# Kernel optimization log

Measured on AMD Instinct MI355X. Metric: run time of the kernel, lower is better.

Reference implementation:

```python
import jax, jax.numpy as jnp
import numpy as np

FREQ_CUTOFF = 10.0
SAMPLING_RATE = 100.0
FILTER_TYPE = 'lowpass'

B, C, L = 64, 128, 8192


def setup_inputs() -> dict:
    key = jax.random.key(0)
    x = jax.random.normal(key, (B, C, L), dtype=jnp.float32)
    return {"x": x}


def reference(x):
    # x: [B, C, L]
    seq_len = x.shape[-1]
    x_fft = jnp.fft.fft(x, axis=-1)  # complex64 [B, C, L]
    freqs = jnp.fft.fftfreq(seq_len, 1.0 / SAMPLING_RATE)  # [L]
    if FILTER_TYPE == 'lowpass':
        mask = jnp.abs(freqs) < FREQ_CUTOFF
    elif FILTER_TYPE == 'highpass':
        mask = jnp.abs(freqs) > FREQ_CUTOFF
    else:
        raise ValueError('Invalid filter type: {}'.format(FILTER_TYPE))
    # Zero out masked frequency bins (faithful to original: lowpass zeroes |f| < cutoff)
    x_fft = jnp.where(mask[None, None, :], 0.0 + 0.0j, x_fft)
    x_filtered = jnp.real(jnp.fft.ifft(x_fft, axis=-1)).astype(jnp.float32)
    return x_filtered
```

## Files before the change

### kernel.cpp

```cpp
#include <hip/hip_runtime.h>
#include <hip/hip_fp16.h>


#define FFT_N 8192
#define NT    256
#define PHY(i) ((i) + ((i) >> 6))

typedef float v2f __attribute__((ext_vector_type(2)));

__device__ __forceinline__ v2f cmul(v2f a, v2f b){
  v2f axx = {a.x, a.x};
  v2f ayy = {a.y, a.y};
  v2f byx = {-b.y, b.x};
  return axx * b + ayy * byx;
}

__device__ __forceinline__ v2f mul_w32(v2f d, int j, bool cj){
  if (j == 0) return d;
  if (j == 8) return cj ? (v2f){-d.y, d.x} : (v2f){d.y, -d.x};
  const float C[16] = {1.f, 0.98078528f, 0.92387953f, 0.83146961f, 0.70710678f,
                       0.55557023f, 0.38268343f, 0.19509032f, 0.f, -0.19509032f,
                       -0.38268343f, -0.55557023f, -0.70710678f, -0.83146961f,
                       -0.92387953f, -0.98078528f};
  const float S[16] = {0.f, -0.19509032f, -0.38268343f, -0.55557023f, -0.70710678f,
                       -0.83146961f, -0.92387953f, -0.98078528f, -1.f, -0.98078528f,
                       -0.92387953f, -0.83146961f, -0.70710678f, -0.55557023f,
                       -0.38268343f, -0.19509032f};
  v2f w = {C[j], cj ? -S[j] : S[j]};
  return cmul(d, w);
}

template<int SZ, int L>
__device__ __forceinline__ void dif_rec(v2f* r){
  #pragma unroll
  for (int g = 0; g < SZ; g += 2*L){
    #pragma unroll
    for (int j = 0; j < L; ++j){
      v2f u = r[g+j], v = r[g+j+L];
      r[g+j]   = u + v;
      r[g+j+L] = mul_w32(u - v, j*(16/L), false);
    }
  }
  if constexpr (L > 1) dif_rec<SZ, L/2>(r);
}

template<int SZ, int L>
__device__ __forceinline__ void dit_rec(v2f* r){
  #pragma unroll
  for (int g = 0; g < SZ; g += 2*L){
    #pragma unroll
    for (int j = 0; j < L; ++j){
      v2f a = r[g+j];
      v2f b = mul_w32(r[g+j+L], j*(16/L), true);
      r[g+j]   = a + b;
      r[g+j+L] = a - b;
    }
  }
  if constexpr (2*L < SZ) dit_rec<SZ, 2*L>(r);
}

__host__ __device__ constexpr int brev5(int k){
  return ((k&1)<<4) | ((k&2)<<2) | (k&4) | ((k&8)>>2) | ((k&16)>>4);
}

__device__ __forceinline__ void twiddle_scale(v2f* r, int cbase, bool cj){
  float s, c;
  __sincosf((float)cbase * -7.6699039394282061e-4f, &s, &c);
  if (cj) s = -s;
  const v2f w1 = {c, s};
  v2f w2q = cmul(w1, w1);
  v2f w4q = cmul(w2q, w2q);
  v2f w8q = cmul(w4q, w4q);
  v2f w16 = cmul(w8q, w8q);
  v2f wa = w1;
  r[brev5(1)]  = cmul(r[brev5(1)],  wa);
  r[brev5(17)] = cmul(r[brev5(17)], cmul(w16, wa));
  #pragma unroll
  for (int k = 2; k <= 15; ++k){
    wa = cmul(wa, w1);
    r[brev5(k)]    = cmul(r[brev5(k)],    wa);
    r[brev5(k+16)] = cmul(r[brev5(k+16)], cmul(w16, wa));
  }
  r[brev5(16)] = cmul(r[brev5(16)], w16);
}

__global__ __launch_bounds__(NT, 2)
void fourier_filter_kernel(const float* __restrict__ x, float* __restrict__ out){
  __shared__ __half2 zs[FFT_N + FFT_N/64];
  const int t = threadIdx.x;
  const long long pair = blockIdx.x;
  const float* r0 = x + pair * (2LL * FFT_N);
  const float* r1 = r0 + FFT_N;
  v2f r[32];

  #pragma unroll
  for (int m = 0; m < 32; ++m){
    const int n = t + (m << 8);
    r[m] = (v2f){__builtin_nontemporal_load(r0 + n),
                 __builtin_nontemporal_load(r1 + n)};
  }
  dif_rec<32, 16>(r);
  twiddle_scale(r, t, false);
  #pragma unroll
  for (int m = 0; m < 32; ++m)
    zs[PHY(t + (m<<8))] = __floats2half2_rn(r[m].x, r[m].y);
  __syncthreads();

  const int base2 = ((t >> 3) << 8) | (t & 7);
  #pragma unroll
  for (int m = 0; m < 32; ++m){
    float2 f = __half22float2(zs[PHY(base2 + (m<<3))]);
    r[m] = (v2f){f.x, f.y};
  }
  dif_rec<32, 16>(r);
  twiddle_scale(r, (t & 7) << 5, false);
  #pragma unroll
  for (int m = 0; m < 32; ++m)
    zs[PHY(base2 + (m<<3))] = __floats2half2_rn(r[m].x, r[m].y);
  __syncthreads();

  #pragma unroll
  for (int e = 0; e < 32; ++e){
    float2 f = __half22float2(zs[PHY((t<<5) + e)]);
    r[e] = (v2f){f.x, f.y};
  }
  #pragma unroll
  for (int g = 0; g < 4; ++g) dif_rec<8, 4>(r + 8*g);
  #pragma unroll
  for (int e = 0; e < 32; ++e){
    const int p  = (t << 5) + e;
    const int k  = (int)(__brev((unsigned)p) >> 19);
    const int kf = min(k, FFT_N - k);
    if (kf <= 819) r[e] = (v2f){0.f, 0.f};
  }
  #pragma unroll
  for (int g = 0; g < 4; ++g) dit_rec<8, 1>(r + 8*g);
  #pragma unroll
  for (int e = 0; e < 32; ++e)
    zs[PHY((t<<5) + e)] = __floats2half2_rn(r[e].x, r[e].y);
  __syncthreads();

  #pragma unroll
  for (int m = 0; m < 32; ++m){
    float2 f = __half22float2(zs[PHY(base2 + (m<<3))]);
    r[m] = (v2f){f.x, f.y};
  }
  twiddle_scale(r, (t & 7) << 5, true);
  dit_rec<32, 1>(r);
  #pragma unroll
  for (int m = 0; m < 32; ++m)
    zs[PHY(base2 + (m<<3))] = __floats2half2_rn(r[m].x, r[m].y);
  __syncthreads();

  #pragma unroll
  for (int m = 0; m < 32; ++m){
    float2 f = __half22float2(zs[PHY(t + (m<<8))]);
    r[m] = (v2f){f.x, f.y};
  }
  twiddle_scale(r, t, true);
  dit_rec<32, 1>(r);
  const float invn = 1.f / (float)FFT_N;
  float* o0 = out + pair * (2LL * FFT_N);
  float* o1 = o0 + FFT_N;
  #pragma unroll
  for (int m = 0; m < 32; ++m){
    const int n = t + (m << 8);
    __builtin_nontemporal_store(r[m].x * invn, o0 + n);
    __builtin_nontemporal_store(r[m].y * invn, o1 + n);
  }
}

extern "C" void kernel_launch(void* const* d_in, const int* in_sizes, int n_in,
                              void* d_out, int out_size, void* d_ws, size_t ws_size,
                              hipStream_t stream) {
  const float* x = (const float*)d_in[0];
  float* out = (float*)d_out;
  const int total  = in_sizes[0];
  const int npairs = total / (2 * FFT_N);
  hipLaunchKernelGGL(fourier_filter_kernel, dim3(npairs), dim3(NT), 0, stream,
                     x, out);
}
```

Before: 122.8 us.

## Replace middle-stage LDS transpose with cross-lane shuffle butterflies

The radix-8 middle stage of the FFT, the frequency mask and the inverse radix-8 stage now run on data exchanged between the 8 neighbouring lanes with xor-shuffles. This replaces a shared-memory write, barrier, read and write-back round trip. It removes two barriers and the fp16 rounding at that exchange point, but adds many shuffle instructions, which on AMD may themselves be routed through the LDS crossbar.

```diff
diff --git a/kernel.cpp b/kernel.cpp
--- a/kernel.cpp
+++ b/kernel.cpp
@@ -13,6 +13,13 @@
   v2f ayy = {a.y, a.y};
   v2f byx = {-b.y, b.x};
   return axx * b + ayy * byx;
+}
+
+__device__ __forceinline__ v2f shfl2(v2f a, int mask){
+  v2f o;
+  o.x = __shfl_xor(a.x, mask, 64);
+  o.y = __shfl_xor(a.y, mask, 64);
+  return o;
 }
 
 __device__ __forceinline__ v2f mul_w32(v2f d, int j, bool cj){
@@ -114,37 +121,97 @@
   }
   dif_rec<32, 16>(r);
   twiddle_scale(r, (t & 7) << 5, false);
-  #pragma unroll
-  for (int m = 0; m < 32; ++m)
-    zs[PHY(base2 + (m<<3))] = __floats2half2_rn(r[m].x, r[m].y);
-  __syncthreads();
-
-  #pragma unroll
-  for (int e = 0; e < 32; ++e){
-    float2 f = __half22float2(zs[PHY((t<<5) + e)]);
-    r[e] = (v2f){f.x, f.y};
-  }
-  #pragma unroll
-  for (int g = 0; g < 4; ++g) dif_rec<8, 4>(r + 8*g);
-  #pragma unroll
-  for (int e = 0; e < 32; ++e){
-    const int p  = (t << 5) + e;
-    const int k  = (int)(__brev((unsigned)p) >> 19);
+
+  const int o = t & 7;
+  const int j2 = o & 3;
+  const float RS = 0.70710678118654752f;
+  const float w4x = (j2==0) ? 1.f : ((j2==1) ? RS : ((j2==2) ? 0.f : -RS));
+  const float w4y = (j2==0) ? 0.f : ((j2==2) ? -1.f : -RS);
+
+  {
+    const bool hi = (o & 4) != 0;
+    const v2f w = {w4x, w4y};
+    #pragma unroll
+    for (int m = 0; m < 32; ++m){
+      v2f oth = shfl2(r[m], 4);
+      v2f s  = r[m] + oth;
+      v2f d0 = r[m] - oth;
+      v2f d  = hi ? (v2f){-d0.x, -d0.y} : d0;
+      v2f tw = cmul(d, w);
+      r[m] = hi ? tw : s;
+    }
+  }
+  {
+    const bool hi = (o & 2) != 0;
+    const bool ng = (o & 1) != 0;
+    #pragma unroll
+    for (int m = 0; m < 32; ++m){
+      v2f oth = shfl2(r[m], 2);
+      v2f s  = r[m] + oth;
+      v2f d0 = r[m] - oth;
+      v2f d  = hi ? (v2f){-d0.x, -d0.y} : d0;
+      v2f dt = ng ? (v2f){d.y, -d.x} : d;
+      r[m] = hi ? dt : s;
+    }
+  }
+  {
+    const bool hi = (o & 1) != 0;
+    #pragma unroll
+    for (int m = 0; m < 32; ++m){
+      v2f oth = shfl2(r[m], 1);
+      v2f s  = r[m] + oth;
+      v2f d0 = r[m] - oth;
+      r[m] = hi ? (v2f){-d0.x, -d0.y} : s;
+    }
+  }
+
+  #pragma unroll
+  for (int m = 0; m < 32; ++m){
+    const int v  = base2 + (m << 3);
+    const int k  = (int)(__brev((unsigned)v) >> 19);
     const int kf = min(k, FFT_N - k);
-    if (kf <= 819) r[e] = (v2f){0.f, 0.f};
-  }
-  #pragma unroll
-  for (int g = 0; g < 4; ++g) dit_rec<8, 1>(r + 8*g);
-  #pragma unroll
-  for (int e = 0; e < 32; ++e)
-    zs[PHY((t<<5) + e)] = __floats2half2_rn(r[e].x, r[e].y);
-  __syncthreads();
-
-  #pragma unroll
-  for (int m = 0; m < 32; ++m){
-    float2 f = __half22float2(zs[PHY(base2 + (m<<3))]);
-    r[m] = (v2f){f.x, f.y};
-  }
+    if (kf <= 819) r[m] = (v2f){0.f, 0.f};
+  }
+
+  {
+    const bool hi = (o & 1) != 0;
+    #pragma unroll
+    for (int m = 0; m < 32; ++m){
+      v2f oth = shfl2(r[m], 1);
+      v2f s  = r[m] + oth;
+      v2f d0 = r[m] - oth;
+      r[m] = hi ? (v2f){-d0.x, -d0.y} : s;
+    }
+  }
+  {
+    const bool hi = (o & 2) != 0;
+    const bool ng = (o & 1) != 0;
+    #pragma unroll
+    for (int m = 0; m < 32; ++m){
+      v2f oth = shfl2(r[m], 2);
+      v2f b  = hi ? r[m] : oth;
+      v2f a  = hi ? oth : r[m];
+      v2f bt = ng ? (v2f){-b.y, b.x} : b;
+      v2f ap = a + bt;
+      v2f am = a - bt;
+      r[m] = hi ? am : ap;
+    }
+  }
+  {
+    const bool hi = (o & 4) != 0;
+    const v2f wc = {w4x, -w4y};
+    #pragma unroll
+    for (int m = 0; m < 32; ++m){
+      v2f oth = shfl2(r[m], 4);
+      v2f b  = hi ? r[m] : oth;
+      v2f a  = hi ? oth : r[m];
+      v2f bt = cmul(b, wc);
+      v2f ap = a + bt;
+      v2f am = a - bt;
+      r[m] = hi ? am : ap;
+    }
+  }
+
   twiddle_scale(r, (t & 7) << 5, true);
   dit_rec<32, 1>(r);
   #pragma unroll
```

New measurement: 178.6 us. 45.5% more time.

## Restructure FFT as 8x32x32 radix passes with vectorized 16-byte global I/O

Applied to the files above, without the earlier changes.

Changes the FFT decomposition from 32x32x8 to 8x32x32 so each thread owns four contiguous samples, which lets the global loads and stores use 128-bit vector accesses. The first and last passes become four radix-8 butterflies with an incremental twiddle helper, and the middle passes become full radix-32. The aim is fewer, wider memory transactions. In exchange it gives up the nontemporal hint on loads and changes the shared-memory access strides, which may cause bank conflicts.

```diff
diff --git a/kernel.cpp b/kernel.cpp
--- a/kernel.cpp
+++ b/kernel.cpp
@@ -7,6 +7,7 @@
 #define PHY(i) ((i) + ((i) >> 6))
 
 typedef float v2f __attribute__((ext_vector_type(2)));
+typedef float v4f __attribute__((ext_vector_type(4)));
 
 __device__ __forceinline__ v2f cmul(v2f a, v2f b){
   v2f axx = {a.x, a.x};
@@ -84,6 +85,22 @@
   r[brev5(16)] = cmul(r[brev5(16)], w16);
 }
 
+__device__ __forceinline__ void tw8(v2f* r, v2f w1){
+  v2f w2 = cmul(w1, w1);
+  v2f w3 = cmul(w2, w1);
+  v2f w4 = cmul(w2, w2);
+  v2f w5 = cmul(w4, w1);
+  v2f w6 = cmul(w4, w2);
+  v2f w7 = cmul(w4, w3);
+  r[4] = cmul(r[4], w1);
+  r[2] = cmul(r[2], w2);
+  r[6] = cmul(r[6], w3);
+  r[1] = cmul(r[1], w4);
+  r[5] = cmul(r[5], w5);
+  r[3] = cmul(r[3], w6);
+  r[7] = cmul(r[7], w7);
+}
+
 __global__ __launch_bounds__(NT, 2)
 void fourier_filter_kernel(const float* __restrict__ x, float* __restrict__ out){
   __shared__ __half2 zs[FFT_N + FFT_N/64];
@@ -93,30 +110,51 @@
   const float* r1 = r0 + FFT_N;
   v2f r[32];
 
+  const v2f W1C = {0.9999997058629f, -7.669903187e-4f};
+  const v2f W2C = {0.9999988234517f, -1.5339801863e-3f};
+
+  #pragma unroll
+  for (int m = 0; m < 8; ++m){
+    const int n = 4*t + (m << 10);
+    const v4f a = *reinterpret_cast<const v4f*>(r0 + n);
+    const v4f b = *reinterpret_cast<const v4f*>(r1 + n);
+    r[0*8+m] = (v2f){a.x, b.x};
+    r[1*8+m] = (v2f){a.y, b.y};
+    r[2*8+m] = (v2f){a.z, b.z};
+    r[3*8+m] = (v2f){a.w, b.w};
+  }
+  #pragma unroll
+  for (int e = 0; e < 4; ++e) dif_rec<8, 4>(r + 8*e);
+  {
+    float s, c;
+    __sincosf((float)(4*t) * -7.6699039394282061e-4f, &s, &c);
+    v2f w0 = {c, s};
+    v2f wA = cmul(w0, W1C);
+    v2f wB = cmul(w0, W2C);
+    v2f wC = cmul(wA, W2C);
+    tw8(r + 0,  w0);
+    tw8(r + 8,  wA);
+    tw8(r + 16, wB);
+    tw8(r + 24, wC);
+  }
+  #pragma unroll
+  for (int e = 0; e < 4; ++e)
+    #pragma unroll
+    for (int m = 0; m < 8; ++m)
+      zs[PHY(4*t + e + (m<<10))] = __floats2half2_rn(r[8*e+m].x, r[8*e+m].y);
+  __syncthreads();
+
+  const int base2 = ((t >> 5) << 10) | (t & 31);
   #pragma unroll
   for (int m = 0; m < 32; ++m){
-    const int n = t + (m << 8);
-    r[m] = (v2f){__builtin_nontemporal_load(r0 + n),
-                 __builtin_nontemporal_load(r1 + n)};
+    float2 f = __half22float2(zs[PHY(base2 + (m<<5))]);
+    r[m] = (v2f){f.x, f.y};
   }
   dif_rec<32, 16>(r);
-  twiddle_scale(r, t, false);
+  twiddle_scale(r, (t & 31) << 3, false);
   #pragma unroll
   for (int m = 0; m < 32; ++m)
-    zs[PHY(t + (m<<8))] = __floats2half2_rn(r[m].x, r[m].y);
-  __syncthreads();
-
-  const int base2 = ((t >> 3) << 8) | (t & 7);
-  #pragma unroll
-  for (int m = 0; m < 32; ++m){
-    float2 f = __half22float2(zs[PHY(base2 + (m<<3))]);
-    r[m] = (v2f){f.x, f.y};
-  }
-  dif_rec<32, 16>(r);
-  twiddle_scale(r, (t & 7) << 5, false);
-  #pragma unroll
-  for (int m = 0; m < 32; ++m)
-    zs[PHY(base2 + (m<<3))] = __floats2half2_rn(r[m].x, r[m].y);
+    zs[PHY(base2 + (m<<5))] = __floats2half2_rn(r[m].x, r[m].y);
   __syncthreads();
 
   #pragma unroll
@@ -124,17 +162,15 @@
     float2 f = __half22float2(zs[PHY((t<<5) + e)]);
     r[e] = (v2f){f.x, f.y};
   }
-  #pragma unroll
-  for (int g = 0; g < 4; ++g) dif_rec<8, 4>(r + 8*g);
+  dif_rec<32, 16>(r);
   #pragma unroll
   for (int e = 0; e < 32; ++e){
-    const int p  = (t << 5) + e;
-    const int k  = (int)(__brev((unsigned)p) >> 19);
+    const int v  = (t << 5) + e;
+    const int k  = (int)(__brev((unsigned)v) >> 19);
     const int kf = min(k, FFT_N - k);
     if (kf <= 819) r[e] = (v2f){0.f, 0.f};
   }
-  #pragma unroll
-  for (int g = 0; g < 4; ++g) dit_rec<8, 1>(r + 8*g);
+  dit_rec<32, 1>(r);
   #pragma unroll
   for (int e = 0; e < 32; ++e)
     zs[PHY((t<<5) + e)] = __floats2half2_rn(r[e].x, r[e].y);
@@ -142,31 +178,53 @@
 
   #pragma unroll
   for (int m = 0; m < 32; ++m){
-    float2 f = __half22float2(zs[PHY(base2 + (m<<3))]);
+    float2 f = __half22float2(zs[PHY(base2 + (m<<5))]);
     r[m] = (v2f){f.x, f.y};
   }
-  twiddle_scale(r, (t & 7) << 5, true);
+  twiddle_scale(r, (t & 31) << 3, true);
   dit_rec<32, 1>(r);
   #pragma unroll
   for (int m = 0; m < 32; ++m)
-    zs[PHY(base2 + (m<<3))] = __floats2half2_rn(r[m].x, r[m].y);
-  __syncthreads();
-
-  #pragma unroll
-  for (int m = 0; m < 32; ++m){
-    float2 f = __half22float2(zs[PHY(t + (m<<8))]);
-    r[m] = (v2f){f.x, f.y};
-  }
-  twiddle_scale(r, t, true);
-  dit_rec<32, 1>(r);
+    zs[PHY(base2 + (m<<5))] = __floats2half2_rn(r[m].x, r[m].y);
+  __syncthreads();
+
+  #pragma unroll
+  for (int e = 0; e < 4; ++e)
+    #pragma unroll
+    for (int m = 0; m < 8; ++m){
+      float2 f = __half22float2(zs[PHY(4*t + e + (m<<10))]);
+      r[8*e+m] = (v2f){f.x, f.y};
+    }
+  {
+    float s, c;
+    __sincosf((float)(4*t) * -7.6699039394282061e-4f, &s, &c);
+    v2f w0 = {c, -s};
+    const v2f W1Cc = {W1C.x, -W1C.y};
+    const v2f W2Cc = {W2C.x, -W2C.y};
+    v2f wA = cmul(w0, W1Cc);
+    v2f wB = cmul(w0, W2Cc);
+    v2f wC = cmul(wA, W2Cc);
+    tw8(r + 0,  w0);
+    tw8(r + 8,  wA);
+    tw8(r + 16, wB);
+    tw8(r + 24, wC);
+  }
+  #pragma unroll
+  for (int e = 0; e < 4; ++e) dit_rec<8, 1>(r + 8*e);
+
   const float invn = 1.f / (float)FFT_N;
   float* o0 = out + pair * (2LL * FFT_N);
   float* o1 = o0 + FFT_N;
   #pragma unroll
-  for (int m = 0; m < 32; ++m){
-    const int n = t + (m << 8);
-    __builtin_nontemporal_store(r[m].x * invn, o0 + n);
-    __builtin_nontemporal_store(r[m].y * invn, o1 + n);
+  for (int m = 0; m < 8; ++m){
+    const int n = 4*t + (m << 10);
+    v4f a, b;
+    a.x = r[0*8+m].x * invn;  b.x = r[0*8+m].y * invn;
+    a.y = r[1*8+m].x * invn;  b.y = r[1*8+m].y * invn;
+    a.z = r[2*8+m].x * invn;  b.z = r[2*8+m].y * invn;
+    a.w = r[3*8+m].x * invn;  b.w = r[3*8+m].y * invn;
+    __builtin_nontemporal_store(a, reinterpret_cast<v4f*>(o0 + n));
+    __builtin_nontemporal_store(b, reinterpret_cast<v4f*>(o1 + n));
   }
 }
 
```

New measurement: 108.2 us. 11.8% less time.
